# Optimization experiments

Hardware: AMD Instinct MI355X
Metric: run time of the kernel (lower is better)

## Reference

```python
import jax, jax.numpy as jnp
import numpy as np

N_NODES = 50000
D_FEAT = 128
N_EDGES = 1_600_000
NUM_ITERATIONS = 20  # init kwarg num_iterations


def setup_inputs() -> dict:
    key = jax.random.key(0)
    k1, k2, k3 = jax.random.split(key, 3)
    x = jax.random.normal(k1, (N_NODES, D_FEAT), dtype=jnp.float32)
    edge_index = jax.random.randint(k2, (2, N_EDGES), 0, N_NODES, dtype=jnp.int32)
    mask = jax.random.bernoulli(k3, 0.5, (N_NODES, D_FEAT))  # True where feature is known
    return {"x": x, "edge_index": edge_index, "mask": mask}


def reference(x, edge_index, mask):
    row, col = edge_index[0], edge_index[1]
    # D^-1/2 A D^-1/2 edge weights (degree computed over col, as in the torch code)
    deg = jax.ops.segment_sum(jnp.ones((N_EDGES,), x.dtype), col, num_segments=N_NODES)
    deg_inv_sqrt = jnp.where(deg > 0, jax.lax.rsqrt(deg), 0.0)
    w = deg_inv_sqrt[row] * deg_inv_sqrt[col]  # [n_edges]

    out0 = jnp.where(mask, x, 0.0)  # zero out unknown features

    def body(_, out):
        # SpMM: result[i] = sum over edges e with row[e]==i of w[e] * out[col[e]]
        msg = w[:, None] * out[col]  # [n_edges, d]
        out = jax.ops.segment_sum(msg, row, num_segments=N_NODES)
        return jnp.where(mask, x, out)  # reset known features each iteration

    return jax.lax.fori_loop(0, NUM_ITERATIONS, body, out0)
```

## Files before the change

### kernel.cpp

```cpp
#include <hip/hip_runtime.h>

#define N_NODES 50000
#define D_FEAT 128
#define N_EDGES 1600000
#define NUM_ITERS 20
#define ZERO_NODE N_NODES
#define HNB 128
#define HALF_NODES 25000
#define NB 196
#define BCAP 192
#define ABLK 128
#define PAD 16
#define STAGE_CAP 12544
#define CSR_MAX (N_EDGES + PAD * N_NODES)

typedef unsigned int u32;
typedef unsigned short u16;
typedef unsigned long long u64;

__device__ __forceinline__ u16 bf16_rne(float f) {
    u32 u = __float_as_uint(f);
    u32 r = u + 0x7fffu + ((u >> 16) & 1u);
    return (u16)(r >> 16);
}

__global__ void detect_kernel(const u32* __restrict__ w, int nwords,
                              u32* __restrict__ flags) {
    int i = blockIdx.x * blockDim.x + threadIdx.x;
    int stride = gridDim.x * blockDim.x;
    u32 f = 0;
    for (; i < nwords; i += stride) {
        u32 v = w[i];
        if (v > 1u) f |= 1u;
        if (v == 0x3f800000u) f |= 2u;
    }
    if (f) atomicOr(flags, f);
}

__global__ void __launch_bounds__(256) hist_kernel(const int* __restrict__ idx,
                                                   u32* __restrict__ partial, int half, int n) {
    __shared__ u32 h[HALF_NODES / 2];
    for (int i = threadIdx.x; i < HALF_NODES / 2; i += 256) h[i] = 0;
    __syncthreads();
    const int base_node = half * HALF_NODES;
    int i = blockIdx.x * 256 + threadIdx.x;
    int stride = gridDim.x * 256;
    for (; i < n; i += stride) {
        u32 r = (u32)(idx[i] - base_node);
        if (r < (u32)HALF_NODES) atomicAdd(&h[r >> 1], 1u << ((r & 1) * 16));
    }
    __syncthreads();
    u32* dst = partial + (size_t)blockIdx.x * (N_NODES / 2) + half * (HALF_NODES / 2);
    for (int j = threadIdx.x; j < HALF_NODES / 2; j += 256) dst[j] = h[j];
}

__global__ void reduce_dis_kernel(const u32* __restrict__ pA, float* __restrict__ dis) {
    int i = blockIdx.x * blockDim.x + threadIdx.x;
    if (i >= N_NODES / 2) return;
    u32 sa = 0;
    for (int b = 0; b < HNB; ++b) sa += pA[(size_t)b * (N_NODES / 2) + i];
    int d0 = (int)(sa & 0xffffu), d1 = (int)(sa >> 16);
    dis[2 * i]     = d0 ? rsqrtf((float)d0) : 0.0f;
    dis[2 * i + 1] = d1 ? rsqrtf((float)d1) : 0.0f;
}

__global__ void __launch_bounds__(256) bucketA_kernel(const int* __restrict__ row,
                                                      const int* __restrict__ col,
                                                      u32* __restrict__ bucket,
                                                      int* __restrict__ bcnt) {
    __shared__ u32 cur[NB];
    for (int i = threadIdx.x; i < NB; i += 256) cur[i] = 0;
    __syncthreads();
    u32* myreg = bucket + (size_t)blockIdx.x * NB * BCAP;
    int i = blockIdx.x * 256 + threadIdx.x;
    int stride = gridDim.x * 256;
    for (; i < N_EDGES; i += stride) {
        int r = row[i];
        int b = r >> 8;
        u32 pos = atomicAdd(&cur[b], 1u);
        if (pos < (u32)BCAP)
            myreg[(size_t)b * BCAP + pos] = ((u32)(r & 255) << 16) | (u32)col[i];
    }
    __syncthreads();
    for (int i2 = threadIdx.x; i2 < NB; i2 += 256)
        bcnt[blockIdx.x * NB + i2] = (int)min(cur[i2], (u32)BCAP);
}

__global__ void __launch_bounds__(256) b1_kernel(const u32* __restrict__ bucket,
                                                 const int* __restrict__ bcnt,
                                                 int* __restrict__ cnt_p) {
    const int b = blockIdx.x;
    const int tid = threadIdx.x;
    __shared__ int pfx[ABLK + 1];
    __shared__ int cnts[ABLK];
    __shared__ u32 hist[256];
    if (tid < 256) hist[tid] = 0;
    if (tid < ABLK) cnts[tid] = bcnt[tid * NB + b];
    __syncthreads();
    if (tid == 0) {
        int s = 0;
        for (int k = 0; k < ABLK; ++k) { pfx[k] = s; s += cnts[k]; }
        pfx[ABLK] = s;
    }
    __syncthreads();
    const int total = pfx[ABLK];
    for (int t = tid; t < total; t += 256) {
        int lo = 0, hi = ABLK;
        while (hi - lo > 1) { int mid = (lo + hi) >> 1; if (pfx[mid] <= t) lo = mid; else hi = mid; }
        u32 e = bucket[(size_t)lo * NB * BCAP + (size_t)b * BCAP + (t - pfx[lo])];
        atomicAdd(&hist[e >> 16], 1u);
    }
    __syncthreads();
    const int r0 = b << 8;
    if (tid < 256) {
        int r = r0 + tid;
        if (r < N_NODES) cnt_p[r] = ((int)hist[tid] + (PAD - 1)) & ~(PAD - 1);
    }
}

__global__ void __launch_bounds__(1024) scan_kernel(const int* __restrict__ cnt,
                                                    int* __restrict__ offsets, int n) {
    __shared__ int wsum[16];
    __shared__ int s_carry;
    const int tid = threadIdx.x;
    const int lane = tid & 63, wid = tid >> 6;
    if (tid == 0) s_carry = 0;
    __syncthreads();
    for (int base = 0; base < n; base += 4096) {
        int i4 = base + tid * 4;
        int4 v = make_int4(0, 0, 0, 0);
        if (i4 < n) v = *(const int4*)(cnt + i4);
        int e1 = v.x, e2 = v.x + v.y, e3 = e2 + v.z, tot = e3 + v.w;
        int winc = tot;
        #pragma unroll
        for (int off = 1; off < 64; off <<= 1) {
            int t = __shfl_up(winc, off);
            if (lane >= off) winc += t;
        }
        if (lane == 63) wsum[wid] = winc;
        __syncthreads();
        if (tid < 16) {
            int s = wsum[tid];
            #pragma unroll
            for (int off = 1; off < 16; off <<= 1) {
                int t = __shfl_up(s, off);
                if (tid >= off) s += t;
            }
            wsum[tid] = s;
        }
        __syncthreads();
        int bb = s_carry + (wid ? wsum[wid - 1] : 0) + winc - tot;
        if (i4 < n) *(int4*)(offsets + i4) = make_int4(bb, bb + e1, bb + e2, bb + e3);
        __syncthreads();
        if (tid == 0) s_carry += wsum[15];
        __syncthreads();
    }
    if (tid == 0) offsets[n] = s_carry;
}

__global__ void __launch_bounds__(256) b2_kernel(const u32* __restrict__ bucket,
                                                 const int* __restrict__ bcnt,
                                                 const int* __restrict__ offsets,
                                                 u16* __restrict__ csr) {
    const int b = blockIdx.x;
    const int tid = threadIdx.x;
    const int r0 = b << 8;
    const int rcount = min(256, N_NODES - r0);
    __shared__ int pfx[ABLK + 1];
    __shared__ int cnts[ABLK];
    __shared__ int lbase[257];
    __shared__ u32 lcur[256];
    __shared__ __align__(16) u16 stage[STAGE_CAP];
    if (tid < ABLK) cnts[tid] = bcnt[tid * NB + b];
    for (int j = tid; j <= rcount; j += 256) lbase[j] = offsets[r0 + j] - offsets[r0];
    if (tid < 256) lcur[tid] = 0;
    __syncthreads();
    if (tid == 0) {
        int s = 0;
        for (int k = 0; k < ABLK; ++k) { pfx[k] = s; s += cnts[k]; }
        pfx[ABLK] = s;
    }
    __syncthreads();
    const int total = pfx[ABLK];
    const int L = min(lbase[rcount], STAGE_CAP);
    for (int j = tid; j < L; j += 256) stage[j] = (u16)ZERO_NODE;
    __syncthreads();
    for (int t = tid; t < total; t += 256) {
        int lo = 0, hi = ABLK;
        while (hi - lo > 1) { int mid = (lo + hi) >> 1; if (pfx[mid] <= t) lo = mid; else hi = mid; }
        u32 e = bucket[(size_t)lo * NB * BCAP + (size_t)b * BCAP + (t - pfx[lo])];
        int lr = (int)(e >> 16);
        u32 p = atomicAdd(&lcur[lr], 1u);
        int idx = lbase[lr] + (int)p;
        if (idx < STAGE_CAP) stage[idx] = (u16)(e & 0xffffu);
    }
    __syncthreads();
    uint4* dst = (uint4*)(csr + offsets[r0]);
    const uint4* src = (const uint4*)stage;
    for (int j = tid; j < (L >> 3); j += 256) dst[j] = src[j];
}

__global__ void build_kernel(const void* __restrict__ mask,
                             const u32* __restrict__ flags,
                             const float* __restrict__ x,
                             const float* __restrict__ dis,
                             u32* __restrict__ bits,
                             u16* __restrict__ sxm, int n) {
    int i = blockIdx.x * blockDim.x + threadIdx.x;
    if (i >= n) return;
    u32 fl = *flags;
    int mv;
    if ((fl & 1u) == 0u) {
        mv = ((const int*)mask)[i];
    } else if (fl & 2u) {
        mv = (((const float*)mask)[i] != 0.0f) ? 1 : 0;
    } else {
        mv = ((const unsigned char*)mask)[i];
    }
    bool pred = (mv != 0);
    u64 b = __ballot(pred);
    int lane = threadIdx.x & 63;
    if (lane == 0)  bits[i >> 5] = (u32)b;
    if (lane == 32) bits[i >> 5] = (u32)(b >> 32);
    sxm[i] = pred ? bf16_rne(dis[i >> 7] * x[i]) : (u16)0;
}

template <bool FINAL>
__global__ void __launch_bounds__(256) prop_kernel(const int* __restrict__ offsets,
                                                   const u16* __restrict__ csr,
                                                   const u16* __restrict__ cur,
                                                   const u32* __restrict__ bits,
                                                   const float* __restrict__ dis,
                                                   const u16* __restrict__ sxm,
                                                   const float* __restrict__ x,
                                                   void* __restrict__ nxtp) {
    const int tid = threadIdx.x;
    const int wid = tid >> 6, lane = tid & 63;
    const int node = blockIdx.x * 4 + wid;
    if (node >= N_NODES) return;
    const int fl = lane & 15, eg = lane >> 4;
    const int s = offsets[node], e = offsets[node + 1];

    float a0 = 0, a1 = 0, a2 = 0, a3 = 0, a4 = 0, a5 = 0, a6 = 0, a7 = 0;
#define ACC(r) \
    a0 += __uint_as_float((r).x << 16); \
    a1 += __uint_as_float((r).x & 0xffff0000u); \
    a2 += __uint_as_float((r).y << 16); \
    a3 += __uint_as_float((r).y & 0xffff0000u); \
    a4 += __uint_as_float((r).z << 16); \
    a5 += __uint_as_float((r).z & 0xffff0000u); \
    a6 += __uint_as_float((r).w << 16); \
    a7 += __uint_as_float((r).w & 0xffff0000u);

    #pragma unroll 2
    for (int base = s; base < e; base += 16) {
        const int c0 = (int)csr[base + eg];
        const int c1 = (int)csr[base + 4 + eg];
        const int c2 = (int)csr[base + 8 + eg];
        const int c3 = (int)csr[base + 12 + eg];
        const uint4 r0 = *((const uint4*)(cur + (size_t)c0 * D_FEAT) + fl);
        const uint4 r1 = *((const uint4*)(cur + (size_t)c1 * D_FEAT) + fl);
        const uint4 r2 = *((const uint4*)(cur + (size_t)c2 * D_FEAT) + fl);
        const uint4 r3 = *((const uint4*)(cur + (size_t)c3 * D_FEAT) + fl);
        ACC(r0); ACC(r1); ACC(r2); ACC(r3);
    }
#undef ACC
    a0 += __shfl_xor(a0, 16); a0 += __shfl_xor(a0, 32);
    a1 += __shfl_xor(a1, 16); a1 += __shfl_xor(a1, 32);
    a2 += __shfl_xor(a2, 16); a2 += __shfl_xor(a2, 32);
    a3 += __shfl_xor(a3, 16); a3 += __shfl_xor(a3, 32);
    a4 += __shfl_xor(a4, 16); a4 += __shfl_xor(a4, 32);
    a5 += __shfl_xor(a5, 16); a5 += __shfl_xor(a5, 32);
    a6 += __shfl_xor(a6, 16); a6 += __shfl_xor(a6, 32);
    a7 += __shfl_xor(a7, 16); a7 += __shfl_xor(a7, 32);

    if (eg == 0) {
        const int fbase = node * D_FEAT + fl * 8;
        const u32 mb = (bits[node * 4 + (fl >> 2)] >> ((fl & 3) * 8)) & 0xffu;
        const float dr = dis[node];
        if (FINAL) {
            const float4 x0 = *(const float4*)(x + fbase);
            const float4 x1 = *(const float4*)(x + fbase + 4);
            float* outp = (float*)nxtp;
            float4 o0, o1;
            o0.x = (mb & 0x01u) ? x0.x : dr * a0;
            o0.y = (mb & 0x02u) ? x0.y : dr * a1;
            o0.z = (mb & 0x04u) ? x0.z : dr * a2;
            o0.w = (mb & 0x08u) ? x0.w : dr * a3;
            o1.x = (mb & 0x10u) ? x1.x : dr * a4;
            o1.y = (mb & 0x20u) ? x1.y : dr * a5;
            o1.z = (mb & 0x40u) ? x1.z : dr * a6;
            o1.w = (mb & 0x80u) ? x1.w : dr * a7;
            *(float4*)(outp + fbase) = o0;
            *(float4*)(outp + fbase + 4) = o1;
        } else {
            const float d2 = dr * dr;
            const uint4 sv = *(const uint4*)(sxm + fbase);
            u16 t0 = (mb & 0x01u) ? (u16)(sv.x)       : bf16_rne(d2 * a0);
            u16 t1 = (mb & 0x02u) ? (u16)(sv.x >> 16) : bf16_rne(d2 * a1);
            u16 t2 = (mb & 0x04u) ? (u16)(sv.y)       : bf16_rne(d2 * a2);
            u16 t3 = (mb & 0x08u) ? (u16)(sv.y >> 16) : bf16_rne(d2 * a3);
            u16 t4 = (mb & 0x10u) ? (u16)(sv.z)       : bf16_rne(d2 * a4);
            u16 t5 = (mb & 0x20u) ? (u16)(sv.z >> 16) : bf16_rne(d2 * a5);
            u16 t6 = (mb & 0x40u) ? (u16)(sv.w)       : bf16_rne(d2 * a6);
            u16 t7 = (mb & 0x80u) ? (u16)(sv.w >> 16) : bf16_rne(d2 * a7);
            uint4 st;
            st.x = (u32)t0 | ((u32)t1 << 16);
            st.y = (u32)t2 | ((u32)t3 << 16);
            st.z = (u32)t4 | ((u32)t5 << 16);
            st.w = (u32)t6 | ((u32)t7 << 16);
            *(uint4*)(((u16*)nxtp) + fbase) = st;
        }
    }
}

extern "C" void kernel_launch(void* const* d_in, const int* in_sizes, int n_in,
                              void* d_out, int out_size, void* d_ws, size_t ws_size,
                              hipStream_t stream) {
    const float* x = (const float*)d_in[0];
    const int* edge = (const int*)d_in[1];
    const void* mask = d_in[2];
    const int* row = edge;
    const int* col = edge + N_EDGES;
    float* out = (float*)d_out;

    char* ws = (char*)d_ws;
    size_t off = 0;
    auto alloc = [&](size_t bytes) -> void* {
        void* p = ws + off;
        off += (bytes + 255) & ~(size_t)255;
        return p;
    };
    const size_t state_elems = (size_t)(N_NODES + 1) * D_FEAT;
    int*   offsets = (int*)alloc((size_t)(N_NODES + 1) * 4);
    int*   cnt_p   = (int*)alloc((size_t)N_NODES * 4);
    float* dis     = (float*)alloc((size_t)N_NODES * 4);
    u32*   flags   = (u32*)alloc(256);
    u32*   bits    = (u32*)alloc((size_t)N_NODES * D_FEAT / 8);
    u32*   pA      = (u32*)alloc((size_t)HNB * (N_NODES / 2) * 4);
    u32*   bucket  = (u32*)alloc((size_t)ABLK * NB * BCAP * 4);
    int*   bcnt    = (int*)alloc((size_t)ABLK * NB * 4);
    u16*   csr     = (u16*)alloc((size_t)CSR_MAX * 2);
    u16*   sxm     = (u16*)alloc(state_elems * 2);
    u16*   stA     = (u16*)alloc(state_elems * 2);
    u16*   stB     = (u16*)alloc(state_elems * 2);

    hipMemsetAsync(flags, 0, 4, stream);
    hipMemsetAsync(sxm + (size_t)N_NODES * D_FEAT, 0, D_FEAT * 2, stream);
    hipMemsetAsync(stA + (size_t)N_NODES * D_FEAT, 0, D_FEAT * 2, stream);
    hipMemsetAsync(stB + (size_t)N_NODES * D_FEAT, 0, D_FEAT * 2, stream);

    const int total_feat = N_NODES * D_FEAT;
    const int mask_words = total_feat / 4;

    detect_kernel<<<1024, 256, 0, stream>>>((const u32*)mask, mask_words, flags);
    hist_kernel<<<HNB, 256, 0, stream>>>(col, pA, 0, N_EDGES);
    hist_kernel<<<HNB, 256, 0, stream>>>(col, pA, 1, N_EDGES);
    reduce_dis_kernel<<<(N_NODES / 2 + 255) / 256, 256, 0, stream>>>(pA, dis);
    bucketA_kernel<<<ABLK, 256, 0, stream>>>(row, col, bucket, bcnt);
    b1_kernel<<<NB, 256, 0, stream>>>(bucket, bcnt, cnt_p);
    scan_kernel<<<1, 1024, 0, stream>>>(cnt_p, offsets, N_NODES);
    build_kernel<<<total_feat / 256, 256, 0, stream>>>(mask, flags, x, dis, bits, sxm, total_feat);
    b2_kernel<<<NB, 256, 0, stream>>>(bucket, bcnt, offsets, csr);

    const int prop_blocks = (N_NODES + 3) / 4;
    const u16* src = sxm;
    for (int it = 0; it < NUM_ITERS; ++it) {
        if (it < NUM_ITERS - 1) {
            u16* dst = (it & 1) ? stB : stA;
            prop_kernel<false><<<prop_blocks, 256, 0, stream>>>(offsets, csr, src, bits, dis, sxm, x, dst);
            src = dst;
        } else {
            prop_kernel<true><<<prop_blocks, 256, 0, stream>>>(offsets, csr, src, bits, dis, sxm, x, out);
        }
    }
}
```

Before: 1.109 ms.

## Pad CSR rows to 4 instead of 16 and sort neighbor indices per row

Reduces the per-row padding granularity of the CSR from 16 to 4 entries, so the gather loop processes 4 edges per step and fetches far fewer dummy zero-node rows. It also insertion-sorts each row's column indices in shared memory during CSR construction, which should improve locality of the gathered feature rows. A tail copy handles staged lengths that are no longer multiples of 8. The serial per-thread insertion sort adds setup cost, and the narrower loop gives less memory-level parallelism per iteration.

```diff
diff --git a/kernel.cpp b/kernel.cpp
--- a/kernel.cpp
+++ b/kernel.cpp
@@ -10,7 +10,7 @@
 #define NB 196
 #define BCAP 192
 #define ABLK 128
-#define PAD 16
+#define PAD 4
 #define STAGE_CAP 12544
 #define CSR_MAX (N_EDGES + PAD * N_NODES)
 
@@ -195,9 +195,28 @@
         if (idx < STAGE_CAP) stage[idx] = (u16)(e & 0xffffu);
     }
     __syncthreads();
+    if (tid < rcount) {
+        const int beg = lbase[tid];
+        const int cnt = (int)lcur[tid];
+        for (int i = 1; i < cnt; ++i) {
+            u16 key = stage[beg + i];
+            int j = i - 1;
+            while (j >= 0 && stage[beg + j] > key) {
+                stage[beg + j + 1] = stage[beg + j];
+                --j;
+            }
+            stage[beg + j + 1] = key;
+        }
+    }
+    __syncthreads();
     uint4* dst = (uint4*)(csr + offsets[r0]);
     const uint4* src = (const uint4*)stage;
     for (int j = tid; j < (L >> 3); j += 256) dst[j] = src[j];
+    if (tid == 0 && (L & 7)) {
+        uint2* d2 = (uint2*)(csr + offsets[r0] + (L & ~7));
+        const uint2* s2 = (const uint2*)(stage + (L & ~7));
+        *d2 = *s2;
+    }
 }
 
 __global__ void build_kernel(const void* __restrict__ mask,
@@ -242,29 +261,19 @@
     const int s = offsets[node], e = offsets[node + 1];
 
     float a0 = 0, a1 = 0, a2 = 0, a3 = 0, a4 = 0, a5 = 0, a6 = 0, a7 = 0;
-#define ACC(r) \
-    a0 += __uint_as_float((r).x << 16); \
-    a1 += __uint_as_float((r).x & 0xffff0000u); \
-    a2 += __uint_as_float((r).y << 16); \
-    a3 += __uint_as_float((r).y & 0xffff0000u); \
-    a4 += __uint_as_float((r).z << 16); \
-    a5 += __uint_as_float((r).z & 0xffff0000u); \
-    a6 += __uint_as_float((r).w << 16); \
-    a7 += __uint_as_float((r).w & 0xffff0000u);
-
-    #pragma unroll 2
-    for (int base = s; base < e; base += 16) {
-        const int c0 = (int)csr[base + eg];
-        const int c1 = (int)csr[base + 4 + eg];
-        const int c2 = (int)csr[base + 8 + eg];
-        const int c3 = (int)csr[base + 12 + eg];
-        const uint4 r0 = *((const uint4*)(cur + (size_t)c0 * D_FEAT) + fl);
-        const uint4 r1 = *((const uint4*)(cur + (size_t)c1 * D_FEAT) + fl);
-        const uint4 r2 = *((const uint4*)(cur + (size_t)c2 * D_FEAT) + fl);
-        const uint4 r3 = *((const uint4*)(cur + (size_t)c3 * D_FEAT) + fl);
-        ACC(r0); ACC(r1); ACC(r2); ACC(r3);
-    }
-#undef ACC
+    #pragma unroll 4
+    for (int base = s; base < e; base += 4) {
+        const int c = (int)csr[base + eg];
+        const uint4 r = *((const uint4*)(cur + (size_t)c * D_FEAT) + fl);
+        a0 += __uint_as_float(r.x << 16);
+        a1 += __uint_as_float(r.x & 0xffff0000u);
+        a2 += __uint_as_float(r.y << 16);
+        a3 += __uint_as_float(r.y & 0xffff0000u);
+        a4 += __uint_as_float(r.z << 16);
+        a5 += __uint_as_float(r.z & 0xffff0000u);
+        a6 += __uint_as_float(r.w << 16);
+        a7 += __uint_as_float(r.w & 0xffff0000u);
+    }
     a0 += __shfl_xor(a0, 16); a0 += __shfl_xor(a0, 32);
     a1 += __shfl_xor(a1, 16); a1 += __shfl_xor(a1, 32);
     a2 += __shfl_xor(a2, 16); a2 += __shfl_xor(a2, 32);
```

After: 1.237 ms. 11.6% more time.
